# Performance work log

Measured on AMD Instinct MI355X. Metric: run time of the kernel, lower is better.

## Reference

```python
import jax, jax.numpy as jnp
import numpy as np

N, E, G = 20000, 320000, 64
H, NF, EF, L, Z = 280, 5, 4, 3, 64
BN_EPS = 1e-5


def _bn(x, g, b):
    # BatchNorm1d in training mode: batch stats over dim 0, biased variance
    m = x.mean(0)
    v = x.var(0)
    return g * (x - m) * jax.lax.rsqrt(v + BN_EPS) + b


def _mlp(x, W1, b1, g1, be1, W2, b2, g2, be2):
    h = jax.nn.relu(_bn(x @ W1 + b1, g1, be1))
    return jax.nn.relu(_bn(h @ W2 + b2, g2, be2))


def setup_inputs() -> dict:
    key = jax.random.key(0)
    ks = jax.random.split(key, 24)
    s = 0.05
    inp = {
        "x": jax.random.normal(ks[0], (N, NF), jnp.float32),
        "edge_attr": jax.random.normal(ks[1], (E, EF), jnp.float32),
        "edge_index": jax.random.randint(ks[2], (2, E), 0, N),
        "batch": jnp.sort(jax.random.randint(ks[3], (N,), 0, G)),
        # input layer
        "Wi": jax.random.normal(ks[4], (NF, H), jnp.float32) * s,
        "bi": jnp.zeros((H,), jnp.float32),
        # message MLP (stacked over L layers): in = 2H+EF
        "Wm1": jax.random.normal(ks[5], (L, 2 * H + EF, H), jnp.float32) * s,
        "bm1": jnp.zeros((L, H), jnp.float32),
        "g1": jnp.ones((L, H), jnp.float32),
        "be1": jnp.zeros((L, H), jnp.float32),
        "Wm2": jax.random.normal(ks[6], (L, H, H), jnp.float32) * s,
        "bm2": jnp.zeros((L, H), jnp.float32),
        "g2": jnp.ones((L, H), jnp.float32),
        "be2": jnp.zeros((L, H), jnp.float32),
        # update MLP: in = 2H
        "Wu1": jax.random.normal(ks[7], (L, 2 * H, H), jnp.float32) * s,
        "bu1": jnp.zeros((L, H), jnp.float32),
        "g3": jnp.ones((L, H), jnp.float32),
        "be3": jnp.zeros((L, H), jnp.float32),
        "Wu2": jax.random.normal(ks[8], (L, H, H), jnp.float32) * s,
        "bu2": jnp.zeros((L, H), jnp.float32),
        "g4": jnp.ones((L, H), jnp.float32),
        "be4": jnp.zeros((L, H), jnp.float32),
        # mu head
        "Wmu": jax.random.normal(ks[9], (H, Z), jnp.float32) * s,
        "bmu": jnp.zeros((Z,), jnp.float32),
    }
    return inp


def reference(x, edge_attr, Wi, bi, Wm1, bm1, g1, be1, Wm2, bm2, g2, be2,
              Wu1, bu1, g3, be3, Wu2, bu2, g4, be4, Wmu, bmu,
              edge_index, batch):
    src, dst = edge_index[0], edge_index[1]
    h = x @ Wi + bi  # [N, H]
    for l in range(L):
        # message: cat(h_i=h[dst], h_j=h[src], edge_attr) -> MLP -> [E, H]
        msg_in = jnp.concatenate([h[dst], h[src], edge_attr], axis=-1)
        msg = _mlp(msg_in, Wm1[l], bm1[l], g1[l], be1[l], Wm2[l], bm2[l], g2[l], be2[l])
        # aggregate: scatter-add into target nodes
        agg = jax.ops.segment_sum(msg, dst, num_segments=N)
        # update: cat(h, agg) -> MLP; residual in GNNEncoder
        upd = _mlp(jnp.concatenate([h, agg], axis=-1),
                   Wu1[l], bu1[l], g3[l], be3[l], Wu2[l], bu2[l], g4[l], be4[l])
        h = h + upd
    # global mean pool over graphs
    sums = jax.ops.segment_sum(h, batch, num_segments=G)
    cnt = jax.ops.segment_sum(jnp.ones((h.shape[0],), h.dtype), batch, num_segments=G)
    pooled = sums / jnp.maximum(cnt, 1.0)[:, None]
    return pooled @ Wmu + bmu  # [G, Z]
```

## Files before the change

### kernel.cpp

```cpp
#include <hip/hip_runtime.h>
#include <hip/hip_bf16.h>

#define NN 20000
#define EE 320000
#define GG 64
#define HH 280
#define NFF 5
#define EFF 4
#define LL 3
#define ZZ 64
#define BN_EPS 1e-5f

typedef __hip_bfloat16 bf;
typedef unsigned short ush;
typedef __attribute__((ext_vector_type(8))) short v8s;
typedef __attribute__((ext_vector_type(4))) float v4f;

__device__ __forceinline__ float us2f(ush u) {
  return __uint_as_float(((unsigned)u) << 16);
}
__device__ __forceinline__ ush f2us(float v) {
  bf b = __float2bfloat16(v);
  return *reinterpret_cast<ush*>(&b);
}
__device__ __forceinline__ int clampi(int v, int hi) {
  return v < 0 ? 0 : (v >= hi ? hi - 1 : v);
}

__global__ void probe_k(const void* __restrict__ x, int* __restrict__ flag) {
  __shared__ int sh[256];
  int tid = threadIdx.x;
  int cnt = 0;
  for (int i = tid; i < 2048; i += 256) {
    ush w = ((const ush*)x)[i];
    unsigned e = (w >> 7) & 0xFF;
    if (w != 0 && (e < 87 || e > 167)) cnt++;
  }
  sh[tid] = cnt;
  __syncthreads();
  for (int o = 128; o > 0; o >>= 1) {
    if (tid < o) sh[tid] += sh[tid + o];
    __syncthreads();
  }
  if (tid == 0) *flag = (sh[0] > 64) ? 1 : 0;
}

__global__ void convert_k(const void* __restrict__ src, float* __restrict__ dst,
                          int n, const int* __restrict__ flag) {
  int i = blockIdx.x * 256 + threadIdx.x;
  if (i < n) {
    if (*flag)
      dst[i] = ((const float*)src)[i];
    else
      dst[i] = us2f(((const ush*)src)[i]);
  }
}

__global__ void wt_ab_k(const float* __restrict__ W, ush* __restrict__ O) {
  int i = blockIdx.x * 256 + threadIdx.x;
  if (i >= 3 * 576 * 288) return;
  int l = i / 165888, r = i % 165888;
  int n = r / 288, k = r % 288;
  float v = 0.f;
  if (n < 560 && k < 280)
    v = (n < 280) ? W[(size_t)l * 157920 + (size_t)k * 280 + n]
                  : W[(size_t)l * 157920 + (size_t)(280 + k) * 280 + (n - 280)];
  O[i] = f2us(v);
}
__global__ void wt_sq_k(const float* __restrict__ W, ush* __restrict__ O) {
  int i = blockIdx.x * 256 + threadIdx.x;
  if (i >= 3 * 320 * 288) return;
  int l = i / 92160, r = i % 92160;
  int n = r / 288, k = r % 288;
  float v = (n < 280 && k < 280) ? W[(size_t)l * 78400 + (size_t)k * 280 + n] : 0.f;
  O[i] = f2us(v);
}
__global__ void wt_u1_k(const float* __restrict__ W, ush* __restrict__ O) {
  int i = blockIdx.x * 256 + threadIdx.x;
  if (i >= 3 * 320 * 576) return;
  int l = i / 184320, r = i % 184320;
  int n = r / 576, k = r % 576;
  float v = (n < 280 && k < 560) ? W[(size_t)l * 156800 + (size_t)k * 280 + n] : 0.f;
  O[i] = f2us(v);
}

struct MG {
  const ush* A;
  const ush* Bt;
  const float* bias;
  void* C;
  float* stats;
  int M, K, Nn, lda, ldb, ldc;
};

template <int CB, int ST>
__global__ __launch_bounds__(256) void mgemm_k(MG g) {
  __shared__ ush Bs[64][296];
  auto red = (float(*)[64])Bs;
  int t = threadIdx.x;
  int n0 = blockIdx.x * 64, m0 = blockIdx.y * 128;
  int lane = t & 63, wv = t >> 6;
  int lrow = lane & 15, quad = lane >> 4;
  int br = t >> 2;
  int bc = (t & 3) * 72;
  v4f acc[2][4];
#pragma unroll
  for (int gi = 0; gi < 2; ++gi)
#pragma unroll
    for (int ci = 0; ci < 4; ++ci) acc[gi][ci] = (v4f){0.f, 0.f, 0.f, 0.f};

  const ush* Arow[2];
  bool av[2];
#pragma unroll
  for (int gi = 0; gi < 2; ++gi) {
    int gm = m0 + (wv << 5) + (gi << 4) + lrow;
    av[gi] = gm < g.M;
    Arow[gi] = g.A + (size_t)gm * g.lda + (quad << 3);
  }
  const ush* Brow = g.Bt + (size_t)(n0 + br) * g.ldb + bc;
  uint4 zz = {0, 0, 0, 0};

  int ntile = g.K / 288;
  for (int tile = 0; tile < ntile; ++tile) {
    int k0 = tile * 288;
    uint4 aR[2][9];
#pragma unroll
    for (int kt = 0; kt < 9; ++kt)
#pragma unroll
      for (int gi = 0; gi < 2; ++gi)
        aR[gi][kt] =
            av[gi] ? *(const uint4*)(Arow[gi] + k0 + (kt << 5)) : zz;
    if (tile) __syncthreads();
#pragma unroll
    for (int i = 0; i < 9; ++i)
      *(uint4*)&Bs[br][bc + (i << 3)] = *(const uint4*)(Brow + k0 + (i << 3));
    __syncthreads();
#pragma unroll
    for (int kt = 0; kt < 9; ++kt) {
      v8s bq[4];
#pragma unroll
      for (int ci = 0; ci < 4; ++ci)
        bq[ci] = *(const v8s*)&Bs[(ci << 4) + lrow][(kt << 5) + (quad << 3)];
#pragma unroll
      for (int gi = 0; gi < 2; ++gi) {
        v8s af = *(v8s*)&aR[gi][kt];
#pragma unroll
        for (int ci = 0; ci < 4; ++ci)
          acc[gi][ci] = __builtin_amdgcn_mfma_f32_16x16x32_bf16(
              af, bq[ci], acc[gi][ci], 0, 0, 0);
      }
    }
  }

  float bj[4];
#pragma unroll
  for (int ci = 0; ci < 4; ++ci) {
    int gn = n0 + (ci << 4) + lrow;
    bj[ci] = (g.bias && gn < g.Nn) ? g.bias[gn] : 0.f;
  }
#pragma unroll
  for (int gi = 0; gi < 2; ++gi)
#pragma unroll
    for (int ci = 0; ci < 4; ++ci)
#pragma unroll
      for (int r = 0; r < 4; ++r) {
        int gm = m0 + (wv << 5) + (gi << 4) + (quad << 2) + r;
        int gn = n0 + (ci << 4) + lrow;
        float v = acc[gi][ci][r] + bj[ci];
        bool ok = (gm < g.M) && (gn < g.Nn);
        if (ok) {
          size_t idx = (size_t)gm * g.ldc + gn;
          if (CB)
            ((ush*)g.C)[idx] = f2us(v);
          else
            ((float*)g.C)[idx] = v;
        }
        acc[gi][ci][r] = ok ? v : 0.f;
      }
  if (ST) {
    int rowg = (wv << 2) | quad;
    __syncthreads();
#pragma unroll
    for (int ci = 0; ci < 4; ++ci) {
      float s = 0.f;
#pragma unroll
      for (int gi = 0; gi < 2; ++gi)
#pragma unroll
        for (int r = 0; r < 4; ++r) s += acc[gi][ci][r];
      red[rowg][(ci << 4) | lrow] = s;
    }
    __syncthreads();
    if (t < 64) {
      float s = 0.f;
#pragma unroll
      for (int r = 0; r < 16; ++r) s += red[r][t];
      int gn = n0 + t;
      if (gn < g.Nn) atomicAdd(&g.stats[gn], s);
    }
    __syncthreads();
#pragma unroll
    for (int ci = 0; ci < 4; ++ci) {
      float s = 0.f;
#pragma unroll
      for (int gi = 0; gi < 2; ++gi)
#pragma unroll
        for (int r = 0; r < 4; ++r) s += acc[gi][ci][r] * acc[gi][ci][r];
      red[rowg][(ci << 4) | lrow] = s;
    }
    __syncthreads();
    if (t < 64) {
      float s = 0.f;
#pragma unroll
      for (int r = 0; r < 16; ++r) s += red[r][t];
      int gn = n0 + t;
      if (gn < g.Nn) atomicAdd(&g.stats[HH + gn], s);
    }
  }
}

__global__ __launch_bounds__(256) void gemm_small_k(
    const float* __restrict__ A, const float* __restrict__ B,
    const float* __restrict__ bias, void* __restrict__ C,
    const int* __restrict__ flag, int M, int K, int Nn, int lda, int ldb,
    int ldc, int outmode) {
  __shared__ alignas(16) float As[16][68];
  __shared__ alignas(16) float Bsm[16][68];
  int tid = threadIdx.x;
  int n0 = blockIdx.x * 64, m0 = blockIdx.y * 64;
  int tx = tid & 15, ty = tid >> 4;
  int am = tid >> 2, akq = (tid & 3) << 2;
  int bk = tid >> 4, bn = (tid & 15) << 2;
  float acc[4][4] = {};
  int gmA = m0 + am;
  int nkt = (K + 15) >> 4;
  for (int kt = 0; kt < nkt; ++kt) {
    int k0 = kt << 4;
#pragma unroll
    for (int i = 0; i < 4; ++i) {
      int gk = k0 + akq + i;
      As[akq + i][am] = (gmA < M && gk < K) ? A[(size_t)gmA * lda + gk] : 0.f;
    }
    {
      int gk = k0 + bk;
      bool kin = gk < K;
#pragma unroll
      for (int j = 0; j < 4; ++j) {
        int gn = n0 + bn + j;
        Bsm[bk][bn + j] = (kin && gn < Nn) ? B[(size_t)gk * ldb + gn] : 0.f;
      }
    }
    __syncthreads();
#pragma unroll
    for (int kk = 0; kk < 16; ++kk) {
      float4 a4 = *(const float4*)&As[kk][ty << 2];
      float4 b4 = *(const float4*)&Bsm[kk][tx << 2];
      float av[4] = {a4.x, a4.y, a4.z, a4.w};
      float bv[4] = {b4.x, b4.y, b4.z, b4.w};
#pragma unroll
      for (int i = 0; i < 4; ++i)
#pragma unroll
        for (int j = 0; j < 4; ++j) acc[i][j] = fmaf(av[i], bv[j], acc[i][j]);
    }
    __syncthreads();
  }
  int ofl = outmode ? *flag : -1;
#pragma unroll
  for (int i = 0; i < 4; ++i) {
    int gm = m0 + (ty << 2) + i;
    if (gm < M) {
#pragma unroll
      for (int j = 0; j < 4; ++j) {
        int gn = n0 + (tx << 2) + j;
        if (gn < Nn) {
          float v = acc[i][j] + (bias ? bias[gn] : 0.f);
          size_t idx = (size_t)gm * ldc + gn;
          if (outmode == 0)
            ((float*)C)[idx] = v;
          else if (ofl)
            ((float*)C)[idx] = v;
          else
            ((ush*)C)[idx] = f2us(v);
        }
      }
    }
  }
}

__global__ __launch_bounds__(256) void edge_stats_k(
    const int* __restrict__ eids, const int* __restrict__ dst,
    const int* __restrict__ src, const float* __restrict__ ea,
    const ush* __restrict__ Pq, const float* __restrict__ W1c,
    const float* __restrict__ b1, float* __restrict__ stats) {
  __shared__ int dstl[256], srcl[256];
  __shared__ float4 eal[256];
  __shared__ float w1cs[4 * HH];
  __shared__ float b1s[HH];
  int tid = threadIdx.x;
  int e0 = blockIdx.x * 256;
  {
    int e = clampi(eids[e0 + tid], EE);
    dstl[tid] = clampi(dst[e], NN);
    srcl[tid] = clampi(src[e], NN);
    eal[tid] = *(const float4*)(ea + (size_t)e * 4);
  }
  for (int i = tid; i < 4 * HH; i += 256) w1cs[i] = W1c[i];
  for (int i = tid; i < HH; i += 256) b1s[i] = b1[i];
  __syncthreads();
  int c0 = tid, c1 = tid + 256;
  bool has1 = c1 < HH;
  float s0 = 0.f, q0 = 0.f, s1 = 0.f, q1 = 0.f;
  for (int e = 0; e < 256; ++e) {
    int d = dstl[e], sn = srcl[e];
    float4 ev = eal[e];
    {
      float raw = us2f(Pq[(size_t)d * 576 + c0]) + us2f(Pq[(size_t)sn * 576 + 280 + c0]);
      float r = ev.x * w1cs[c0] + ev.y * w1cs[HH + c0] +
                ev.z * w1cs[2 * HH + c0] + ev.w * w1cs[3 * HH + c0];
      float tv = raw + r + b1s[c0];
      s0 += tv; q0 += tv * tv;
    }
    if (has1) {
      float raw = us2f(Pq[(size_t)d * 576 + c1]) + us2f(Pq[(size_t)sn * 576 + 280 + c1]);
      float r = ev.x * w1cs[c1] + ev.y * w1cs[HH + c1] +
                ev.z * w1cs[2 * HH + c1] + ev.w * w1cs[3 * HH + c1];
      float tv = raw + r + b1s[c1];
      s1 += tv; q1 += tv * tv;
    }
  }
  atomicAdd(&stats[c0], s0);
  atomicAdd(&stats[HH + c0], q0);
  if (has1) {
    atomicAdd(&stats[c1], s1);
    atomicAdd(&stats[HH + c1], q1);
  }
}

__global__ void bn_finalize_k(const float* __restrict__ stats, float cnt,
                              const float* __restrict__ gw,
                              const float* __restrict__ bw,
                              const float* __restrict__ extra,
                              float* __restrict__ scale,
                              float* __restrict__ shift) {
  int c = threadIdx.x;
  if (c < HH) {
    float m = stats[c] / cnt;
    float v = stats[HH + c] / cnt - m * m;
    v = v < 0.f ? 0.f : v;
    float r = rsqrtf(v + BN_EPS);
    float sc = gw[c] * r;
    float sh = bw[c] - sc * m + (extra ? sc * extra[c] : 0.f);
    scale[c] = sc;
    shift[c] = sh;
  }
}

__global__ void hist_k(const int* __restrict__ dst, int* __restrict__ counts) {
  int e = blockIdx.x * 256 + threadIdx.x;
  if (e < EE) atomicAdd(&counts[clampi(dst[e], NN)], 1);
}

__global__ __launch_bounds__(1024) void scan_k(const int* __restrict__ counts,
                                               int* __restrict__ offs, int n) {
  __shared__ int buf[1024];
  __shared__ int running;
  int tid = threadIdx.x;
  if (tid == 0) running = 0;
  __syncthreads();
  for (int base = 0; base < n; base += 1024) {
    int v = (base + tid < n) ? counts[base + tid] : 0;
    buf[tid] = v;
    __syncthreads();
    for (int off = 1; off < 1024; off <<= 1) {
      int t = (tid >= off) ? buf[tid - off] : 0;
      __syncthreads();
      buf[tid] += t;
      __syncthreads();
    }
    int incl = buf[tid];
    if (base + tid < n) offs[base + tid] = running + incl - v;
    __syncthreads();
    if (tid == 1023) running += incl;
    __syncthreads();
  }
  if (tid == 0) offs[n] = running;
}

__global__ void fill_k(const int* __restrict__ dst, const int* __restrict__ offs,
                       int* __restrict__ cursor, int* __restrict__ eids) {
  int e = blockIdx.x * 256 + threadIdx.x;
  if (e < EE) {
    int n = clampi(dst[e], NN);
    int pos = atomicAdd(&cursor[n], 1);
    int idx = offs[n] + pos;
    if (idx >= 0 && idx < EE) eids[idx] = e;
  }
}

__global__ __launch_bounds__(256) void build_t1_k(
    const int* __restrict__ eids, const int* __restrict__ dst,
    const int* __restrict__ src, const float* __restrict__ ea,
    const ush* __restrict__ Pq, const float* __restrict__ W1c,
    const float* __restrict__ sc, const float* __restrict__ sh,
    ush* __restrict__ T1, int cb) {
  __shared__ float scs[HH], shs[HH], w1[4 * HH];
  int t = threadIdx.x;
  for (int i = t; i < HH; i += 256) { scs[i] = sc[i]; shs[i] = sh[i]; }
  for (int i = t; i < 4 * HH; i += 256) w1[i] = W1c[i];
  __syncthreads();
  int base = blockIdx.x * 32;
  int c2 = t + 256;
  bool h2 = c2 < HH;
  for (int i = 0; i < 32; ++i) {
    int r = cb + base + i;
    int e = clampi(eids[r], EE);
    int d = clampi(dst[e], NN), s = clampi(src[e], NN);
    float4 ev = *(const float4*)(ea + (size_t)e * 4);
    size_t pd = (size_t)d * 576, ps = (size_t)s * 576 + 280;
    size_t orow = (size_t)(base + i) * 288;
    {
      int c = t;
      float v = us2f(Pq[pd + c]) + us2f(Pq[ps + c]) + ev.x * w1[c] +
                ev.y * w1[HH + c] + ev.z * w1[2 * HH + c] + ev.w * w1[3 * HH + c];
      v = fmaf(scs[c], v, shs[c]);
      T1[orow + c] = f2us(v > 0.f ? v : 0.f);
    }
    if (h2) {
      int c = c2;
      float v = us2f(Pq[pd + c]) + us2f(Pq[ps + c]) + ev.x * w1[c] +
                ev.y * w1[HH + c] + ev.z * w1[2 * HH + c] + ev.w * w1[3 * HH + c];
      v = fmaf(scs[c], v, shs[c]);
      T1[orow + c] = f2us(v > 0.f ? v : 0.f);
    }
  }
}

__global__ __launch_bounds__(256) void aggregate_k(
    const int* __restrict__ offs, const ush* __restrict__ tmp2,
    const float* __restrict__ scale, const float* __restrict__ shift,
    float* __restrict__ agg, int e0, int e1) {
  int n = blockIdx.x;
  int rs = offs[n], re = offs[n + 1];
  if (rs < e0) rs = e0;
  if (re > e1) re = e1;
  if (rs >= re) return;
  int t = threadIdx.x;
  int c2 = t + 256;
  bool h2 = c2 < HH;
  float a0 = 0.f, a1 = 0.f;
  float sc0 = scale[t], sh0 = shift[t];
  float sc1 = h2 ? scale[c2] : 0.f, sh1 = h2 ? shift[c2] : 0.f;
  for (int r = rs; r < re; ++r) {
    const ush* row = tmp2 + (size_t)(r - e0) * HH;
    float v0 = fmaf(sc0, us2f(row[t]), sh0);
    a0 += v0 > 0.f ? v0 : 0.f;
    if (h2) {
      float v1 = fmaf(sc1, us2f(row[c2]), sh1);
      a1 += v1 > 0.f ? v1 : 0.f;
    }
  }
  agg[(size_t)n * HH + t] += a0;
  if (h2) agg[(size_t)n * HH + c2] += a1;
}

__global__ void hb_k(const float* __restrict__ h, ush* __restrict__ hcat) {
  int i = blockIdx.x * 256 + threadIdx.x;
  if (i < NN * HH) {
    int n = i / HH, c = i % HH;
    hcat[(size_t)n * 576 + c] = f2us(h[i]);
  }
}
__global__ void agg2hcat_k(const float* __restrict__ agg, ush* __restrict__ hcat) {
  int i = blockIdx.x * 256 + threadIdx.x;
  if (i < NN * HH) {
    int n = i / HH, c = i % HH;
    hcat[(size_t)n * 576 + 280 + c] = f2us(agg[i]);
  }
}
__global__ void u2a_k(const float* __restrict__ u1, const float* __restrict__ sc,
                      const float* __restrict__ sh, ush* __restrict__ u2A) {
  int i = blockIdx.x * 256 + threadIdx.x;
  if (i < NN * HH) {
    int n = i / HH, c = i % HH;
    float v = fmaf(sc[c], u1[i], sh[c]);
    u2A[(size_t)n * 288 + c] = f2us(v > 0.f ? v : 0.f);
  }
}
__global__ void residual_k(float* __restrict__ h, const float* __restrict__ u2,
                           const float* __restrict__ scale,
                           const float* __restrict__ shift) {
  int i = blockIdx.x * 256 + threadIdx.x;
  if (i < NN * HH) {
    int c = i % HH;
    float v = fmaf(scale[c], u2[i], shift[c]);
    h[i] += v > 0.f ? v : 0.f;
  }
}

__device__ __forceinline__ int lowerb(const int* a, int n, int key) {
  int lo = 0, hi = n;
  while (lo < hi) {
    int mid = (lo + hi) >> 1;
    if (a[mid] < key) lo = mid + 1; else hi = mid;
  }
  return lo;
}

__global__ __launch_bounds__(256) void pool_k(const float* __restrict__ h,
                                              const int* __restrict__ batch,
                                              float* __restrict__ pooled) {
  __shared__ float red[4][56];
  int gid = blockIdx.x, cc = blockIdx.y;
  int start = lowerb(batch, NN, gid);
  int end = lowerb(batch, NN, gid + 1);
  int cnt = end - start;
  float inv = 1.f / (float)(cnt > 1 ? cnt : 1);
  int grp = threadIdx.x >> 6, ci = threadIdx.x & 63;
  if (ci < 56) {
    int col = cc * 56 + ci;
    float s = 0.f;
    for (int n = start + grp; n < end; n += 4) s += h[(size_t)n * HH + col];
    red[grp][ci] = s;
  }
  __syncthreads();
  if (threadIdx.x < 56) {
    float s = red[0][threadIdx.x] + red[1][threadIdx.x] +
              red[2][threadIdx.x] + red[3][threadIdx.x];
    pooled[(size_t)gid * HH + cc * 56 + threadIdx.x] = s * inv;
  }
}

extern "C" void kernel_launch(void* const* d_in, const int* in_sizes, int n_in,
                              void* d_out, int out_size, void* d_ws,
                              size_t ws_size, hipStream_t stream) {
  const int* eidx = (const int*)d_in[2];
  const int* batch = (const int*)d_in[3];
  const int* srcp = eidx;
  const int* dstp = eidx + EE;
  size_t NH = (size_t)NN * HH;

  float* w0 = (float*)d_ws;
  size_t off = 0;
  auto alloc = [&](size_t n) {
    float* p = w0 + off;
    off += (n + 3) & ~(size_t)3;
    return p;
  };
  int* flag = (int*)alloc(4);
  float* cx = alloc(100000);
  float* cea = alloc(1280000);
  float* cWi = alloc(1400);
  float* cbi = alloc(280);
  float* cWm1 = alloc(473760);
  float* cbm1 = alloc(840);
  float* cg1 = alloc(840);
  float* cbe1 = alloc(840);
  float* cWm2 = alloc(235200);
  float* cbm2 = alloc(840);
  float* cg2 = alloc(840);
  float* cbe2 = alloc(840);
  float* cWu1 = alloc(470400);
  float* cbu1 = alloc(840);
  float* cg3 = alloc(840);
  float* cbe3 = alloc(840);
  float* cWu2 = alloc(235200);
  float* cbu2 = alloc(840);
  float* cg4 = alloc(840);
  float* cbe4 = alloc(840);
  float* cWmu = alloc(17920);
  float* cbmu = alloc(64);
  ush* W1ab = (ush*)alloc(248832);
  ush* W2t = (ush*)alloc(138240);
  ush* WU1t = (ush*)alloc(276480);
  ush* WU2t = (ush*)alloc(138240);
  float* h = alloc(NH);
  ush* hcat = (ush*)alloc(5824512);
  ush* u2A = hcat;
  float* pqr = alloc(5824512);
  ush* Pq = (ush*)pqr;
  float* u1f = pqr;
  float* agg = alloc(NH);
  float* pooled = alloc((size_t)GG * HH);
  float* stats = alloc(8 * HH);
  float* ss = alloc(8 * HH);
  int* counts = (int*)alloc(NN);
  int* offs = (int*)alloc(NN + 1);
  int* cursor = (int*)alloc(NN);
  int* eids = (int*)alloc(EE);
  size_t baseB = off * 4;

  int EC = 6400, T2 = 6400;
  {
    const int ecs[5] = {64000, 64000, 32000, 12800, 6400};
    const int t2s[5] = {EE, 64000, 32000, 12800, 6400};
    for (int i = 0; i < 5; ++i) {
      size_t need = baseB + (size_t)ecs[i] * 288 * 2 + (size_t)t2s[i] * 280 * 2 + 64;
      if (need <= ws_size) { EC = ecs[i]; T2 = t2s[i]; break; }
    }
  }
  ush* T1c = (ush*)(w0 + off);
  ush* tmp2 = T1c + (size_t)EC * 288;
  bool stored = (T2 == EE);
  int nch = EE / EC;

  probe_k<<<1, 256, 0, stream>>>(d_in[0], flag);
  struct Cv { const void* s; float* d; int n; };
  const Cv cv[22] = {
      {d_in[0], cx, NN * NFF},     {d_in[1], cea, EE * EFF},
      {d_in[4], cWi, NFF * HH},    {d_in[5], cbi, HH},
      {d_in[6], cWm1, LL * (2 * HH + EFF) * HH}, {d_in[7], cbm1, LL * HH},
      {d_in[8], cg1, LL * HH},     {d_in[9], cbe1, LL * HH},
      {d_in[10], cWm2, LL * HH * HH}, {d_in[11], cbm2, LL * HH},
      {d_in[12], cg2, LL * HH},    {d_in[13], cbe2, LL * HH},
      {d_in[14], cWu1, LL * 2 * HH * HH}, {d_in[15], cbu1, LL * HH},
      {d_in[16], cg3, LL * HH},    {d_in[17], cbe3, LL * HH},
      {d_in[18], cWu2, LL * HH * HH}, {d_in[19], cbu2, LL * HH},
      {d_in[20], cg4, LL * HH},    {d_in[21], cbe4, LL * HH},
      {d_in[22], cWmu, HH * ZZ},   {d_in[23], cbmu, ZZ}};
  for (int i = 0; i < 22; ++i)
    convert_k<<<(cv[i].n + 255) / 256, 256, 0, stream>>>(cv[i].s, cv[i].d, cv[i].n, flag);

  wt_ab_k<<<(3 * 576 * 288 + 255) / 256, 256, 0, stream>>>(cWm1, W1ab);
  wt_sq_k<<<(3 * 320 * 288 + 255) / 256, 256, 0, stream>>>(cWm2, W2t);
  wt_u1_k<<<(3 * 320 * 576 + 255) / 256, 256, 0, stream>>>(cWu1, WU1t);
  wt_sq_k<<<(3 * 320 * 288 + 255) / 256, 256, 0, stream>>>(cWu2, WU2t);

  gemm_small_k<<<dim3(5, 313), 256, 0, stream>>>(cx, cWi, cbi, h, nullptr, NN,
                                                 NFF, HH, NFF, HH, HH, 0);
  hipMemsetAsync(counts, 0, NN * sizeof(int), stream);
  hipMemsetAsync(cursor, 0, NN * sizeof(int), stream);
  hist_k<<<(EE + 255) / 256, 256, 0, stream>>>(dstp, counts);
  scan_k<<<1, 1024, 0, stream>>>(counts, offs, NN);
  fill_k<<<(EE + 255) / 256, 256, 0, stream>>>(dstp, offs, cursor, eids);

  int elemGrid = (int)((NH + 255) / 256);
  for (int l = 0; l < LL; ++l) {
    ush* Wab = W1ab + (size_t)l * 576 * 288;
    ush* W2l = W2t + (size_t)l * 320 * 288;
    ush* WU1l = WU1t + (size_t)l * 320 * 576;
    ush* WU2l = WU2t + (size_t)l * 320 * 288;
    const float* W1c = cWm1 + (size_t)l * 157920 + (size_t)560 * 280;
    float* st1 = stats; float* st2 = stats + 560;
    float* st3 = stats + 1120; float* st4 = stats + 1680;
    float* ss1 = ss; float* ss2 = ss + 560;
    float* ss3 = ss + 1120; float* ss4 = ss + 1680;
    hipMemsetAsync(stats, 0, 8 * HH * sizeof(float), stream);

    hb_k<<<elemGrid, 256, 0, stream>>>(h, hcat);
    {
      MG g = {hcat, Wab, nullptr, Pq, nullptr, NN, 288, 560, 576, 288, 576};
      mgemm_k<1, 0><<<dim3(9, 157), 256, 0, stream>>>(g);
    }
    edge_stats_k<<<EE / 256, 256, 0, stream>>>(eids, dstp, srcp, cea, Pq, W1c,
                                               cbm1 + l * HH, st1);
    bn_finalize_k<<<1, 320, 0, stream>>>(st1, (float)EE, cg1 + l * HH,
                                         cbe1 + l * HH, cbm1 + l * HH, ss1, ss1 + HH);
    for (int c = 0; c < nch; ++c) {
      int cb = c * EC;
      build_t1_k<<<EC / 32, 256, 0, stream>>>(eids, dstp, srcp, cea, Pq, W1c,
                                              ss1, ss1 + HH, T1c, cb);
      MG g = {T1c, W2l, cbm2 + l * HH,
              stored ? (void*)(tmp2 + (size_t)cb * HH) : (void*)tmp2, st2,
              EC, 288, HH, 288, 288, HH};
      mgemm_k<1, 1><<<dim3(5, EC / 128), 256, 0, stream>>>(g);
    }
    bn_finalize_k<<<1, 320, 0, stream>>>(st2, (float)EE, cg2 + l * HH,
                                         cbe2 + l * HH, nullptr, ss2, ss2 + HH);
    hipMemsetAsync(agg, 0, NH * sizeof(float), stream);
    if (stored) {
      aggregate_k<<<NN, 256, 0, stream>>>(offs, tmp2, ss2, ss2 + HH, agg, 0, EE);
    } else {
      for (int c = 0; c < nch; ++c) {
        int cb = c * EC;
        build_t1_k<<<EC / 32, 256, 0, stream>>>(eids, dstp, srcp, cea, Pq, W1c,
                                                ss1, ss1 + HH, T1c, cb);
        MG g = {T1c, W2l, cbm2 + l * HH, (void*)tmp2, nullptr,
                EC, 288, HH, 288, 288, HH};
        mgemm_k<1, 0><<<dim3(5, EC / 128), 256, 0, stream>>>(g);
        aggregate_k<<<NN, 256, 0, stream>>>(offs, tmp2, ss2, ss2 + HH, agg, cb, cb + EC);
      }
    }
    agg2hcat_k<<<elemGrid, 256, 0, stream>>>(agg, hcat);
    {
      MG g = {hcat, WU1l, cbu1 + l * HH, u1f, st3, NN, 576, HH, 576, 576, HH};
      mgemm_k<0, 1><<<dim3(5, 157), 256, 0, stream>>>(g);
    }
    bn_finalize_k<<<1, 320, 0, stream>>>(st3, (float)NN, cg3 + l * HH,
                                         cbe3 + l * HH, nullptr, ss3, ss3 + HH);
    u2a_k<<<elemGrid, 256, 0, stream>>>(u1f, ss3, ss3 + HH, u2A);
    {
      MG g = {u2A, WU2t + (size_t)l * 320 * 288, cbu2 + l * HH, agg, st4,
              NN, 288, HH, 288, 288, HH};
      mgemm_k<0, 1><<<dim3(5, 157), 256, 0, stream>>>(g);
    }
    bn_finalize_k<<<1, 320, 0, stream>>>(st4, (float)NN, cg4 + l * HH,
                                         cbe4 + l * HH, nullptr, ss4, ss4 + HH);
    residual_k<<<elemGrid, 256, 0, stream>>>(h, agg, ss4, ss4 + HH);
  }

  pool_k<<<dim3(GG, 5), 256, 0, stream>>>(h, batch, pooled);
  gemm_small_k<<<dim3(1, 1), 256, 0, stream>>>(pooled, cWmu, cbmu, d_out, flag,
                                               GG, HH, ZZ, HH, ZZ, ZZ, 1);
}
```

Measured before the change: 4.275 ms.

## Fold BN finalize into consumers, batch conversions, fuse hcat writes, larger chunks

Removes the separate bn_finalize launches by recomputing the BN scale and shift inline in each consumer kernel. It merges the 22 per-tensor conversion launches and four weight-transpose launches into one launch each. The bf16 hcat copy of h and agg is now written directly by the input GEMM, the residual kernel and the aggregate kernel, which drops hb_k, the agg memset and agg2hcat in the stored path. It also restructures edge_stats to use 128 edges per block with batched gathers and register-held weights, and allows larger edge chunks when the workspace fits. The trade-off is redundant per-thread BN math and a larger workspace footprint.

```diff
diff --git a/kernel.cpp b/kernel.cpp
--- a/kernel.cpp
+++ b/kernel.cpp
@@ -26,6 +26,16 @@
 __device__ __forceinline__ int clampi(int v, int hi) {
   return v < 0 ? 0 : (v >= hi ? hi - 1 : v);
 }
+__device__ __forceinline__ void bnfold(const float* st, int c, float invc,
+                                       const float* gw, const float* bw,
+                                       const float* extra, float& sc,
+                                       float& sh) {
+  float m = st[c] * invc;
+  float v = st[HH + c] * invc - m * m;
+  v = v < 0.f ? 0.f : v;
+  sc = gw[c] * rsqrtf(v + BN_EPS);
+  sh = bw[c] - sc * m + (extra ? sc * extra[c] : 0.f);
+}
 
 __global__ void probe_k(const void* __restrict__ x, int* __restrict__ flag) {
   __shared__ int sh[256];
@@ -45,43 +55,66 @@
   if (tid == 0) *flag = (sh[0] > 64) ? 1 : 0;
 }
 
-__global__ void convert_k(const void* __restrict__ src, float* __restrict__ dst,
-                          int n, const int* __restrict__ flag) {
+struct CvArgs {
+  const void* src[22];
+  float* dst[22];
+  int n[22];
+  int bstart[23];
+};
+__global__ __launch_bounds__(256) void convert_all_k(CvArgs a,
+                                                     const int* __restrict__ flag) {
+  int b = blockIdx.x;
+  int s = 0;
+  while (b >= a.bstart[s + 1]) ++s;
+  int i = (b - a.bstart[s]) * 256 + threadIdx.x;
+  if (i < a.n[s]) {
+    if (*flag)
+      a.dst[s][i] = ((const float*)a.src[s])[i];
+    else
+      a.dst[s][i] = us2f(((const ush*)a.src[s])[i]);
+  }
+}
+
+__global__ __launch_bounds__(256) void wt_all_k(
+    const float* __restrict__ cWm1, const float* __restrict__ cWm2,
+    const float* __restrict__ cWu1, const float* __restrict__ cWu2,
+    ush* __restrict__ W1ab, ush* __restrict__ W2t, ush* __restrict__ WU1t,
+    ush* __restrict__ WU2t) {
   int i = blockIdx.x * 256 + threadIdx.x;
-  if (i < n) {
-    if (*flag)
-      dst[i] = ((const float*)src)[i];
-    else
-      dst[i] = us2f(((const ush*)src)[i]);
-  }
-}
-
-__global__ void wt_ab_k(const float* __restrict__ W, ush* __restrict__ O) {
-  int i = blockIdx.x * 256 + threadIdx.x;
-  if (i >= 3 * 576 * 288) return;
-  int l = i / 165888, r = i % 165888;
-  int n = r / 288, k = r % 288;
-  float v = 0.f;
-  if (n < 560 && k < 280)
-    v = (n < 280) ? W[(size_t)l * 157920 + (size_t)k * 280 + n]
-                  : W[(size_t)l * 157920 + (size_t)(280 + k) * 280 + (n - 280)];
-  O[i] = f2us(v);
-}
-__global__ void wt_sq_k(const float* __restrict__ W, ush* __restrict__ O) {
-  int i = blockIdx.x * 256 + threadIdx.x;
-  if (i >= 3 * 320 * 288) return;
-  int l = i / 92160, r = i % 92160;
-  int n = r / 288, k = r % 288;
-  float v = (n < 280 && k < 280) ? W[(size_t)l * 78400 + (size_t)k * 280 + n] : 0.f;
-  O[i] = f2us(v);
-}
-__global__ void wt_u1_k(const float* __restrict__ W, ush* __restrict__ O) {
-  int i = blockIdx.x * 256 + threadIdx.x;
-  if (i >= 3 * 320 * 576) return;
-  int l = i / 184320, r = i % 184320;
-  int n = r / 576, k = r % 576;
-  float v = (n < 280 && k < 560) ? W[(size_t)l * 156800 + (size_t)k * 280 + n] : 0.f;
-  O[i] = f2us(v);
+  const int nA = 3 * 576 * 288, nB = 3 * 320 * 288, nC = 3 * 320 * 576;
+  if (i < nA) {
+    int l = i / 165888, r = i % 165888;
+    int n = r / 288, k = r % 288;
+    float v = 0.f;
+    if (n < 560 && k < 280)
+      v = (n < 280) ? cWm1[(size_t)l * 157920 + (size_t)k * 280 + n]
+                    : cWm1[(size_t)l * 157920 + (size_t)(280 + k) * 280 + (n - 280)];
+    W1ab[i] = f2us(v);
+    return;
+  }
+  i -= nA;
+  if (i < nB) {
+    int l = i / 92160, r = i % 92160;
+    int n = r / 288, k = r % 288;
+    float v = (n < 280 && k < 280) ? cWm2[(size_t)l * 78400 + (size_t)k * 280 + n] : 0.f;
+    W2t[i] = f2us(v);
+    return;
+  }
+  i -= nB;
+  if (i < nC) {
+    int l = i / 184320, r = i % 184320;
+    int n = r / 576, k = r % 576;
+    float v = (n < 280 && k < 560) ? cWu1[(size_t)l * 156800 + (size_t)k * 280 + n] : 0.f;
+    WU1t[i] = f2us(v);
+    return;
+  }
+  i -= nC;
+  if (i < nB) {
+    int l = i / 92160, r = i % 92160;
+    int n = r / 288, k = r % 288;
+    float v = (n < 280 && k < 280) ? cWu2[(size_t)l * 78400 + (size_t)k * 280 + n] : 0.f;
+    WU2t[i] = f2us(v);
+  }
 }
 
 struct MG {
@@ -128,8 +161,7 @@
     for (int kt = 0; kt < 9; ++kt)
 #pragma unroll
       for (int gi = 0; gi < 2; ++gi)
-        aR[gi][kt] =
-            av[gi] ? *(const uint4*)(Arow[gi] + k0 + (kt << 5)) : zz;
+        aR[gi][kt] = av[gi] ? *(const uint4*)(Arow[gi] + k0 + (kt << 5)) : zz;
     if (tile) __syncthreads();
 #pragma unroll
     for (int i = 0; i < 9; ++i)
@@ -221,8 +253,8 @@
 __global__ __launch_bounds__(256) void gemm_small_k(
     const float* __restrict__ A, const float* __restrict__ B,
     const float* __restrict__ bias, void* __restrict__ C,
-    const int* __restrict__ flag, int M, int K, int Nn, int lda, int ldb,
-    int ldc, int outmode) {
+    const int* __restrict__ flag, ush* __restrict__ hc, int M, int K, int Nn,
+    int lda, int ldb, int ldc, int outmode) {
   __shared__ alignas(16) float As[16][68];
   __shared__ alignas(16) float Bsm[16][68];
   int tid = threadIdx.x;
@@ -274,9 +306,10 @@
         if (gn < Nn) {
           float v = acc[i][j] + (bias ? bias[gn] : 0.f);
           size_t idx = (size_t)gm * ldc + gn;
-          if (outmode == 0)
+          if (outmode == 0) {
             ((float*)C)[idx] = v;
-          else if (ofl)
+            if (hc) hc[(size_t)gm * 576 + gn] = f2us(v);
+          } else if (ofl)
             ((float*)C)[idx] = v;
           else
             ((ush*)C)[idx] = f2us(v);
@@ -291,13 +324,13 @@
     const int* __restrict__ src, const float* __restrict__ ea,
     const ush* __restrict__ Pq, const float* __restrict__ W1c,
     const float* __restrict__ b1, float* __restrict__ stats) {
-  __shared__ int dstl[256], srcl[256];
-  __shared__ float4 eal[256];
+  __shared__ int dstl[128], srcl[128];
+  __shared__ float4 eal[128];
   __shared__ float w1cs[4 * HH];
   __shared__ float b1s[HH];
   int tid = threadIdx.x;
-  int e0 = blockIdx.x * 256;
-  {
+  int e0 = blockIdx.x * 128;
+  if (tid < 128) {
     int e = clampi(eids[e0 + tid], EE);
     dstl[tid] = clampi(dst[e], NN);
     srcl[tid] = clampi(src[e], NN);
@@ -308,23 +341,39 @@
   __syncthreads();
   int c0 = tid, c1 = tid + 256;
   bool has1 = c1 < HH;
+  float w0x = w1cs[c0], w0y = w1cs[HH + c0], w0z = w1cs[2 * HH + c0],
+        w0w = w1cs[3 * HH + c0], b0v = b1s[c0];
+  float w1x = 0, w1y = 0, w1z = 0, w1w = 0, b1v = 0;
+  if (has1) {
+    w1x = w1cs[c1]; w1y = w1cs[HH + c1]; w1z = w1cs[2 * HH + c1];
+    w1w = w1cs[3 * HH + c1]; b1v = b1s[c1];
+  }
   float s0 = 0.f, q0 = 0.f, s1 = 0.f, q1 = 0.f;
-  for (int e = 0; e < 256; ++e) {
-    int d = dstl[e], sn = srcl[e];
-    float4 ev = eal[e];
-    {
-      float raw = us2f(Pq[(size_t)d * 576 + c0]) + us2f(Pq[(size_t)sn * 576 + 280 + c0]);
-      float r = ev.x * w1cs[c0] + ev.y * w1cs[HH + c0] +
-                ev.z * w1cs[2 * HH + c0] + ev.w * w1cs[3 * HH + c0];
-      float tv = raw + r + b1s[c0];
-      s0 += tv; q0 += tv * tv;
-    }
-    if (has1) {
-      float raw = us2f(Pq[(size_t)d * 576 + c1]) + us2f(Pq[(size_t)sn * 576 + 280 + c1]);
-      float r = ev.x * w1cs[c1] + ev.y * w1cs[HH + c1] +
-                ev.z * w1cs[2 * HH + c1] + ev.w * w1cs[3 * HH + c1];
-      float tv = raw + r + b1s[c1];
-      s1 += tv; q1 += tv * tv;
+  for (int e = 0; e < 128; e += 4) {
+    ush pd[4], ps[4], pd2[4], ps2[4];
+#pragma unroll
+    for (int j = 0; j < 4; ++j) {
+      size_t bd = (size_t)dstl[e + j] * 576, bs = (size_t)srcl[e + j] * 576 + 280;
+      pd[j] = Pq[bd + c0];
+      ps[j] = Pq[bs + c0];
+      if (has1) {
+        pd2[j] = Pq[bd + c1];
+        ps2[j] = Pq[bs + c1];
+      }
+    }
+#pragma unroll
+    for (int j = 0; j < 4; ++j) {
+      float4 ev = eal[e + j];
+      float tv = us2f(pd[j]) + us2f(ps[j]) + ev.x * w0x + ev.y * w0y +
+                 ev.z * w0z + ev.w * w0w + b0v;
+      s0 += tv;
+      q0 += tv * tv;
+      if (has1) {
+        float t2 = us2f(pd2[j]) + us2f(ps2[j]) + ev.x * w1x + ev.y * w1y +
+                   ev.z * w1z + ev.w * w1w + b1v;
+        s1 += t2;
+        q1 += t2 * t2;
+      }
     }
   }
   atomicAdd(&stats[c0], s0);
@@ -332,25 +381,6 @@
   if (has1) {
     atomicAdd(&stats[c1], s1);
     atomicAdd(&stats[HH + c1], q1);
-  }
-}
-
-__global__ void bn_finalize_k(const float* __restrict__ stats, float cnt,
-                              const float* __restrict__ gw,
-                              const float* __restrict__ bw,
-                              const float* __restrict__ extra,
-                              float* __restrict__ scale,
-                              float* __restrict__ shift) {
-  int c = threadIdx.x;
-  if (c < HH) {
-    float m = stats[c] / cnt;
-    float v = stats[HH + c] / cnt - m * m;
-    v = v < 0.f ? 0.f : v;
-    float r = rsqrtf(v + BN_EPS);
-    float sc = gw[c] * r;
-    float sh = bw[c] - sc * m + (extra ? sc * extra[c] : 0.f);
-    scale[c] = sc;
-    shift[c] = sh;
   }
 }
 
@@ -400,11 +430,18 @@
     const int* __restrict__ eids, const int* __restrict__ dst,
     const int* __restrict__ src, const float* __restrict__ ea,
     const ush* __restrict__ Pq, const float* __restrict__ W1c,
-    const float* __restrict__ sc, const float* __restrict__ sh,
+    const float* __restrict__ st1, const float* __restrict__ gw,
+    const float* __restrict__ bw, const float* __restrict__ b1,
     ush* __restrict__ T1, int cb) {
   __shared__ float scs[HH], shs[HH], w1[4 * HH];
   int t = threadIdx.x;
-  for (int i = t; i < HH; i += 256) { scs[i] = sc[i]; shs[i] = sh[i]; }
+  const float invE = 1.f / EE;
+  for (int i = t; i < HH; i += 256) {
+    float sc, sh;
+    bnfold(st1, i, invE, gw, bw, b1, sc, sh);
+    scs[i] = sc;
+    shs[i] = sh;
+  }
   for (int i = t; i < 4 * HH; i += 256) w1[i] = W1c[i];
   __syncthreads();
   int base = blockIdx.x * 32;
@@ -436,19 +473,21 @@
 
 __global__ __launch_bounds__(256) void aggregate_k(
     const int* __restrict__ offs, const ush* __restrict__ tmp2,
-    const float* __restrict__ scale, const float* __restrict__ shift,
-    float* __restrict__ agg, int e0, int e1) {
+    const float* __restrict__ st2, const float* __restrict__ gw,
+    const float* __restrict__ bw, float* __restrict__ agg,
+    ush* __restrict__ hcat, int e0, int e1, int accum) {
   int n = blockIdx.x;
+  int t = threadIdx.x;
+  int c2 = t + 256;
+  bool h2 = c2 < HH;
+  const float invE = 1.f / EE;
+  float sc0, sh0, sc1 = 0.f, sh1 = 0.f;
+  bnfold(st2, t, invE, gw, bw, nullptr, sc0, sh0);
+  if (h2) bnfold(st2, c2, invE, gw, bw, nullptr, sc1, sh1);
   int rs = offs[n], re = offs[n + 1];
   if (rs < e0) rs = e0;
   if (re > e1) re = e1;
-  if (rs >= re) return;
-  int t = threadIdx.x;
-  int c2 = t + 256;
-  bool h2 = c2 < HH;
   float a0 = 0.f, a1 = 0.f;
-  float sc0 = scale[t], sh0 = shift[t];
-  float sc1 = h2 ? scale[c2] : 0.f, sh1 = h2 ? shift[c2] : 0.f;
   for (int r = rs; r < re; ++r) {
     const ush* row = tmp2 + (size_t)(r - e0) * HH;
     float v0 = fmaf(sc0, us2f(row[t]), sh0);
@@ -458,17 +497,21 @@
       a1 += v1 > 0.f ? v1 : 0.f;
     }
   }
-  agg[(size_t)n * HH + t] += a0;
-  if (h2) agg[(size_t)n * HH + c2] += a1;
-}
-
-__global__ void hb_k(const float* __restrict__ h, ush* __restrict__ hcat) {
-  int i = blockIdx.x * 256 + threadIdx.x;
-  if (i < NN * HH) {
-    int n = i / HH, c = i % HH;
-    hcat[(size_t)n * 576 + c] = f2us(h[i]);
-  }
-}
+  if (accum) {
+    if (rs < re) {
+      agg[(size_t)n * HH + t] += a0;
+      if (h2) agg[(size_t)n * HH + c2] += a1;
+    }
+  } else {
+    agg[(size_t)n * HH + t] = a0;
+    hcat[(size_t)n * 576 + 280 + t] = f2us(a0);
+    if (h2) {
+      agg[(size_t)n * HH + c2] = a1;
+      hcat[(size_t)n * 576 + 280 + c2] = f2us(a1);
+    }
+  }
+}
+
 __global__ void agg2hcat_k(const float* __restrict__ agg, ush* __restrict__ hcat) {
   int i = blockIdx.x * 256 + threadIdx.x;
   if (i < NN * HH) {
@@ -476,23 +519,34 @@
     hcat[(size_t)n * 576 + 280 + c] = f2us(agg[i]);
   }
 }
-__global__ void u2a_k(const float* __restrict__ u1, const float* __restrict__ sc,
-                      const float* __restrict__ sh, ush* __restrict__ u2A) {
+
+__global__ void u2a_k(const float* __restrict__ u1, const float* __restrict__ st3,
+                      const float* __restrict__ gw, const float* __restrict__ bw,
+                      ush* __restrict__ u2A) {
   int i = blockIdx.x * 256 + threadIdx.x;
   if (i < NN * HH) {
     int n = i / HH, c = i % HH;
-    float v = fmaf(sc[c], u1[i], sh[c]);
+    float sc, sh;
+    bnfold(st3, c, 1.f / NN, gw, bw, nullptr, sc, sh);
+    float v = fmaf(sc, u1[i], sh);
     u2A[(size_t)n * 288 + c] = f2us(v > 0.f ? v : 0.f);
   }
 }
+
 __global__ void residual_k(float* __restrict__ h, const float* __restrict__ u2,
-                           const float* __restrict__ scale,
-                           const float* __restrict__ shift) {
+                           const float* __restrict__ st4,
+                           const float* __restrict__ gw,
+                           const float* __restrict__ bw,
+                           ush* __restrict__ hcat) {
   int i = blockIdx.x * 256 + threadIdx.x;
   if (i < NN * HH) {
-    int c = i % HH;
-    float v = fmaf(scale[c], u2[i], shift[c]);
-    h[i] += v > 0.f ? v : 0.f;
+    int n = i / HH, c = i % HH;
+    float sc, sh;
+    bnfold(st4, c, 1.f / NN, gw, bw, nullptr, sc, sh);
+    float v = fmaf(sc, u2[i], sh);
+    float nh = h[i] + (v > 0.f ? v : 0.f);
+    h[i] = nh;
+    hcat[(size_t)n * 576 + c] = f2us(nh);
   }
 }
 
@@ -581,18 +635,17 @@
   float* agg = alloc(NH);
   float* pooled = alloc((size_t)GG * HH);
   float* stats = alloc(8 * HH);
-  float* ss = alloc(8 * HH);
   int* counts = (int*)alloc(NN);
+  int* cursor = (int*)alloc(NN);
   int* offs = (int*)alloc(NN + 1);
-  int* cursor = (int*)alloc(NN);
   int* eids = (int*)alloc(EE);
   size_t baseB = off * 4;
 
   int EC = 6400, T2 = 6400;
   {
-    const int ecs[5] = {64000, 64000, 32000, 12800, 6400};
-    const int t2s[5] = {EE, 64000, 32000, 12800, 6400};
-    for (int i = 0; i < 5; ++i) {
+    const int ecs[6] = {320000, 160000, 64000, 32000, 12800, 6400};
+    const int t2s[6] = {EE, EE, EE, 32000, 12800, 6400};
+    for (int i = 0; i < 6; ++i) {
       size_t need = baseB + (size_t)ecs[i] * 288 * 2 + (size_t)t2s[i] * 280 * 2 + 64;
       if (need <= ws_size) { EC = ecs[i]; T2 = t2s[i]; break; }
     }
@@ -603,31 +656,40 @@
   int nch = EE / EC;
 
   probe_k<<<1, 256, 0, stream>>>(d_in[0], flag);
-  struct Cv { const void* s; float* d; int n; };
-  const Cv cv[22] = {
-      {d_in[0], cx, NN * NFF},     {d_in[1], cea, EE * EFF},
-      {d_in[4], cWi, NFF * HH},    {d_in[5], cbi, HH},
-      {d_in[6], cWm1, LL * (2 * HH + EFF) * HH}, {d_in[7], cbm1, LL * HH},
-      {d_in[8], cg1, LL * HH},     {d_in[9], cbe1, LL * HH},
-      {d_in[10], cWm2, LL * HH * HH}, {d_in[11], cbm2, LL * HH},
-      {d_in[12], cg2, LL * HH},    {d_in[13], cbe2, LL * HH},
-      {d_in[14], cWu1, LL * 2 * HH * HH}, {d_in[15], cbu1, LL * HH},
-      {d_in[16], cg3, LL * HH},    {d_in[17], cbe3, LL * HH},
-      {d_in[18], cWu2, LL * HH * HH}, {d_in[19], cbu2, LL * HH},
-      {d_in[20], cg4, LL * HH},    {d_in[21], cbe4, LL * HH},
-      {d_in[22], cWmu, HH * ZZ},   {d_in[23], cbmu, ZZ}};
-  for (int i = 0; i < 22; ++i)
-    convert_k<<<(cv[i].n + 255) / 256, 256, 0, stream>>>(cv[i].s, cv[i].d, cv[i].n, flag);
-
-  wt_ab_k<<<(3 * 576 * 288 + 255) / 256, 256, 0, stream>>>(cWm1, W1ab);
-  wt_sq_k<<<(3 * 320 * 288 + 255) / 256, 256, 0, stream>>>(cWm2, W2t);
-  wt_u1_k<<<(3 * 320 * 576 + 255) / 256, 256, 0, stream>>>(cWu1, WU1t);
-  wt_sq_k<<<(3 * 320 * 288 + 255) / 256, 256, 0, stream>>>(cWu2, WU2t);
-
-  gemm_small_k<<<dim3(5, 313), 256, 0, stream>>>(cx, cWi, cbi, h, nullptr, NN,
-                                                 NFF, HH, NFF, HH, HH, 0);
-  hipMemsetAsync(counts, 0, NN * sizeof(int), stream);
-  hipMemsetAsync(cursor, 0, NN * sizeof(int), stream);
+  {
+    CvArgs ca;
+    const void* srcs[22] = {d_in[0],  d_in[1],  d_in[4],  d_in[5],  d_in[6],
+                            d_in[7],  d_in[8],  d_in[9],  d_in[10], d_in[11],
+                            d_in[12], d_in[13], d_in[14], d_in[15], d_in[16],
+                            d_in[17], d_in[18], d_in[19], d_in[20], d_in[21],
+                            d_in[22], d_in[23]};
+    float* dsts[22] = {cx,   cea,  cWi,  cbi,  cWm1, cbm1, cg1,  cbe1,
+                       cWm2, cbm2, cg2,  cbe2, cWu1, cbu1, cg3,  cbe3,
+                       cWu2, cbu2, cg4,  cbe4, cWmu, cbmu};
+    int ns[22] = {NN * NFF, EE * EFF, NFF * HH, HH,
+                  LL * (2 * HH + EFF) * HH, LL * HH, LL * HH, LL * HH,
+                  LL * HH * HH, LL * HH, LL * HH, LL * HH,
+                  LL * 2 * HH * HH, LL * HH, LL * HH, LL * HH,
+                  LL * HH * HH, LL * HH, LL * HH, LL * HH,
+                  HH * ZZ, ZZ};
+    int bs = 0;
+    for (int i = 0; i < 22; ++i) {
+      ca.src[i] = srcs[i];
+      ca.dst[i] = dsts[i];
+      ca.n[i] = ns[i];
+      ca.bstart[i] = bs;
+      bs += (ns[i] + 255) / 256;
+    }
+    ca.bstart[22] = bs;
+    convert_all_k<<<bs, 256, 0, stream>>>(ca, flag);
+  }
+  wt_all_k<<<6264, 256, 0, stream>>>(cWm1, cWm2, cWu1, cWu2, W1ab, W2t, WU1t,
+                                     WU2t);
+
+  gemm_small_k<<<dim3(5, 313), 256, 0, stream>>>(cx, cWi, cbi, h, nullptr,
+                                                 hcat, NN, NFF, HH, NFF, HH,
+                                                 HH, 0);
+  hipMemsetAsync(counts, 0, 2 * NN * sizeof(int), stream);
   hist_k<<<(EE + 255) / 256, 256, 0, stream>>>(dstp, counts);
   scan_k<<<1, 1024, 0, stream>>>(counts, offs, NN);
   fill_k<<<(EE + 255) / 256, 256, 0, stream>>>(dstp, offs, cursor, eids);
@@ -639,65 +701,64 @@
     ush* WU1l = WU1t + (size_t)l * 320 * 576;
     ush* WU2l = WU2t + (size_t)l * 320 * 288;
     const float* W1c = cWm1 + (size_t)l * 157920 + (size_t)560 * 280;
-    float* st1 = stats; float* st2 = stats + 560;
-    float* st3 = stats + 1120; float* st4 = stats + 1680;
-    float* ss1 = ss; float* ss2 = ss + 560;
-    float* ss3 = ss + 1120; float* ss4 = ss + 1680;
+    float* st1 = stats;
+    float* st2 = stats + 560;
+    float* st3 = stats + 1120;
+    float* st4 = stats + 1680;
     hipMemsetAsync(stats, 0, 8 * HH * sizeof(float), stream);
 
-    hb_k<<<elemGrid, 256, 0, stream>>>(h, hcat);
     {
       MG g = {hcat, Wab, nullptr, Pq, nullptr, NN, 288, 560, 576, 288, 576};
       mgemm_k<1, 0><<<dim3(9, 157), 256, 0, stream>>>(g);
     }
-    edge_stats_k<<<EE / 256, 256, 0, stream>>>(eids, dstp, srcp, cea, Pq, W1c,
+    edge_stats_k<<<EE / 128, 256, 0, stream>>>(eids, dstp, srcp, cea, Pq, W1c,
                                                cbm1 + l * HH, st1);
-    bn_finalize_k<<<1, 320, 0, stream>>>(st1, (float)EE, cg1 + l * HH,
-                                         cbe1 + l * HH, cbm1 + l * HH, ss1, ss1 + HH);
     for (int c = 0; c < nch; ++c) {
       int cb = c * EC;
       build_t1_k<<<EC / 32, 256, 0, stream>>>(eids, dstp, srcp, cea, Pq, W1c,
-                                              ss1, ss1 + HH, T1c, cb);
+                                              st1, cg1 + l * HH, cbe1 + l * HH,
+                                              cbm1 + l * HH, T1c, cb);
       MG g = {T1c, W2l, cbm2 + l * HH,
               stored ? (void*)(tmp2 + (size_t)cb * HH) : (void*)tmp2, st2,
               EC, 288, HH, 288, 288, HH};
       mgemm_k<1, 1><<<dim3(5, EC / 128), 256, 0, stream>>>(g);
     }
-    bn_finalize_k<<<1, 320, 0, stream>>>(st2, (float)EE, cg2 + l * HH,
-                                         cbe2 + l * HH, nullptr, ss2, ss2 + HH);
-    hipMemsetAsync(agg, 0, NH * sizeof(float), stream);
     if (stored) {
-      aggregate_k<<<NN, 256, 0, stream>>>(offs, tmp2, ss2, ss2 + HH, agg, 0, EE);
+      aggregate_k<<<NN, 256, 0, stream>>>(offs, tmp2, st2, cg2 + l * HH,
+                                          cbe2 + l * HH, agg, hcat, 0, EE, 0);
     } else {
+      hipMemsetAsync(agg, 0, NH * sizeof(float), stream);
       for (int c = 0; c < nch; ++c) {
         int cb = c * EC;
         build_t1_k<<<EC / 32, 256, 0, stream>>>(eids, dstp, srcp, cea, Pq, W1c,
-                                                ss1, ss1 + HH, T1c, cb);
+                                                st1, cg1 + l * HH,
+                                                cbe1 + l * HH, cbm1 + l * HH,
+                                                T1c, cb);
         MG g = {T1c, W2l, cbm2 + l * HH, (void*)tmp2, nullptr,
                 EC, 288, HH, 288, 288, HH};
         mgemm_k<1, 0><<<dim3(5, EC / 128), 256, 0, stream>>>(g);
-        aggregate_k<<<NN, 256, 0, stream>>>(offs, tmp2, ss2, ss2 + HH, agg, cb, cb + EC);
+        aggregate_k<<<NN, 256, 0, stream>>>(offs, tmp2, st2, cg2 + l * HH,
+                                            cbe2 + l * HH, agg, hcat, cb,
+                                            cb + EC, 1);
       }
-    }
-    agg2hcat_k<<<elemGrid, 256, 0, stream>>>(agg, hcat);
+      agg2hcat_k<<<elemGrid, 256, 0, stream>>>(agg, hcat);
+    }
     {
       MG g = {hcat, WU1l, cbu1 + l * HH, u1f, st3, NN, 576, HH, 576, 576, HH};
       mgemm_k<0, 1><<<dim3(5, 157), 256, 0, stream>>>(g);
     }
-    bn_finalize_k<<<1, 320, 0, stream>>>(st3, (float)NN, cg3 + l * HH,
-                                         cbe3 + l * HH, nullptr, ss3, ss3 + HH);
-    u2a_k<<<elemGrid, 256, 0, stream>>>(u1f, ss3, ss3 + HH, u2A);
+    u2a_k<<<elemGrid, 256, 0, stream>>>(u1f, st3, cg3 + l * HH, cbe3 + l * HH,
+                                        u2A);
     {
-      MG g = {u2A, WU2t + (size_t)l * 320 * 288, cbu2 + l * HH, agg, st4,
-              NN, 288, HH, 288, 288, HH};
+      MG g = {u2A, WU2l, cbu2 + l * HH, agg, st4, NN, 288, HH, 288, 288, HH};
       mgemm_k<0, 1><<<dim3(5, 157), 256, 0, stream>>>(g);
     }
-    bn_finalize_k<<<1, 320, 0, stream>>>(st4, (float)NN, cg4 + l * HH,
-                                         cbe4 + l * HH, nullptr, ss4, ss4 + HH);
-    residual_k<<<elemGrid, 256, 0, stream>>>(h, agg, ss4, ss4 + HH);
+    residual_k<<<elemGrid, 256, 0, stream>>>(h, agg, st4, cg4 + l * HH,
+                                             cbe4 + l * HH, hcat);
   }
 
   pool_k<<<dim3(GG, 5), 256, 0, stream>>>(h, batch, pooled);
   gemm_small_k<<<dim3(1, 1), 256, 0, stream>>>(pooled, cWmu, cbmu, d_out, flag,
-                                               GG, HH, ZZ, HH, ZZ, ZZ, 1);
-}
+                                               nullptr, GG, HH, ZZ, HH, ZZ, ZZ,
+                                               1);
+}
```

After: 5.391 ms. 1.26x slower.
